# Kernel tuning notes

Measured on AMD Instinct MI355X. Metric: run time of the kernel, lower is better.

The kernel has to match this reference:

```python
import jax, jax.numpy as jnp
import numpy as np

BN_EPS = 1e-5


def setup_inputs() -> dict:
    key = jax.random.key(0)
    ks = jax.random.split(key, 16)
    B, n, m, C1, C2 = 8, 8192, 2048, 256, 256
    Cin, H1, H2 = C1 + C2, 512, 512
    inp = {
        'unknown': jax.random.uniform(ks[0], (B, n, 3), jnp.float32),
        'known': jax.random.uniform(ks[1], (B, m, 3), jnp.float32),
        'unknow_feats': jax.random.normal(ks[2], (B, C1, n), jnp.float32),
        'known_feats': jax.random.normal(ks[3], (B, C2, m), jnp.float32),
        # shared-MLP layer 1: Conv2d(512 -> 512, k=1, bias=False) + BN + ReLU
        'W1': jax.random.normal(ks[4], (H1, Cin), jnp.float32) * (1.0 / np.sqrt(Cin)),
        'g1': jax.random.uniform(ks[5], (H1,), jnp.float32, 0.5, 1.5),
        'b1': jax.random.normal(ks[6], (H1,), jnp.float32) * 0.1,
        'm1': jax.random.normal(ks[7], (H1,), jnp.float32) * 0.1,
        'v1': jax.random.uniform(ks[8], (H1,), jnp.float32, 0.5, 1.5),
        # shared-MLP layer 2
        'W2': jax.random.normal(ks[9], (H2, H1), jnp.float32) * (1.0 / np.sqrt(H1)),
        'g2': jax.random.uniform(ks[10], (H2,), jnp.float32, 0.5, 1.5),
        'b2': jax.random.normal(ks[11], (H2,), jnp.float32) * 0.1,
        'm2': jax.random.normal(ks[12], (H2,), jnp.float32) * 0.1,
        'v2': jax.random.uniform(ks[13], (H2,), jnp.float32, 0.5, 1.5),
    }
    return inp


def three_nn(unknown, known):
    # brute-force squared L2 distances (CUDA kernel returns squared dists)
    d2 = jnp.sum((unknown[:, :, None, :] - known[:, None, :, :]) ** 2, axis=-1)  # (B,n,m)
    neg_d, idx = jax.lax.top_k(-d2, 3)  # 3 smallest
    return -neg_d, idx  # (B,n,3), (B,n,3)


def three_interpolate(feats, idx, weight):
    # feats (B,C,m), idx (B,n,3), weight (B,n,3) -> (B,C,n)
    def _one(f, i, w):
        return jnp.einsum('cnk,nk->cn', f[:, i], w)
    return jax.vmap(_one)(feats, idx, weight)


def _conv_bn_relu(x, W, g, b, mu, var):
    # x (B,Cin,n) -> (B,Cout,n); 1x1 conv + inference BatchNorm + ReLU
    y = jnp.einsum('oc,bcn->bon', W, x)
    scale = g / jnp.sqrt(var + BN_EPS)
    y = y * scale[None, :, None] + (b - mu * scale)[None, :, None]
    return jax.nn.relu(y)


def reference(unknown, known, unknow_feats, known_feats,
              W1, g1, b1, m1, v1, W2, g2, b2, m2, v2):
    dist, idx = three_nn(unknown, known)
    dist_recip = 1.0 / (dist + 1e-8)
    weight = dist_recip / jnp.sum(dist_recip, axis=2, keepdims=True)
    new_features = three_interpolate(known_feats, idx, weight)  # (B,C2,n)
    new_features = jnp.concatenate([new_features, unknow_feats], axis=1)  # (B,C1+C2,n)
    h = _conv_bn_relu(new_features, W1, g1, b1, m1, v1)
    out = _conv_bn_relu(h, W2, g2, b2, m2, v2)
    return out  # (B, 512, n)
```

## Files before the change

kernel.cpp:

```cpp
#include <hip/hip_runtime.h>

typedef __bf16 bf16_t;
typedef __bf16 bf16x8 __attribute__((ext_vector_type(8)));
typedef float f32x4 __attribute__((ext_vector_type(4)));

#define AS1 __attribute__((address_space(1)))
#define AS3 __attribute__((address_space(3)))

__device__ __forceinline__ void gload_lds16(const void* g, void* l) {
    __builtin_amdgcn_global_load_lds((const AS1 unsigned int*)g,
                                     (AS3 unsigned int*)l, 16, 0, 0);
}

__device__ __forceinline__ unsigned int pack2(float a, float b) {
    unsigned short lo = __builtin_bit_cast(unsigned short, (bf16_t)a);
    unsigned short hi = __builtin_bit_cast(unsigned short, (bf16_t)b);
    return (unsigned int)lo | ((unsigned int)hi << 16);
}

__global__ __launch_bounds__(256) void prep_all(
    const float* __restrict__ W1, const float* __restrict__ W2,
    bf16_t* __restrict__ Wc1, bf16_t* __restrict__ Wc2,
    const float* g1, const float* b1, const float* m1, const float* v1,
    const float* g2, const float* b2, const float* m2, const float* v2,
    float* s1, float* t1, float* s2, float* t2)
{
    const int bx = blockIdx.x;
    if (bx < 1024) {
        size_t i = (size_t)bx * 256 + threadIdx.x;
        Wc1[i] = (bf16_t)W1[i];
    } else if (bx < 2048) {
        size_t i = (size_t)(bx - 1024) * 256 + threadIdx.x;
        Wc2[i] = (bf16_t)W2[i];
    } else {
#pragma unroll
        for (int k = 0; k < 2; ++k) {
            int i = threadIdx.x + k * 256;
            float s = __fdiv_rn(g1[i], __fsqrt_rn(__fadd_rn(v1[i], 1e-5f)));
            s1[i] = s;
            t1[i] = __fsub_rn(b1[i], __fmul_rn(m1[i], s));
            float q = __fdiv_rn(g2[i], __fsqrt_rn(__fadd_rn(v2[i], 1e-5f)));
            s2[i] = q;
            t2[i] = __fsub_rn(b2[i], __fmul_rn(m2[i], q));
        }
    }
}

__device__ __forceinline__ void insdi(float d, int i,
                                      float& D1, int& I1, float& D2, int& I2,
                                      float& D3, int& I3) {
    const bool q1 = d < D1, q2 = d < D2, q3 = d < D3;
    I3 = q2 ? I2 : (q3 ? i : I3);
    I2 = q1 ? I1 : (q2 ? i : I2);
    I1 = q1 ? i : I1;
    D3 = __builtin_amdgcn_fmed3f(d, D2, D3);
    D2 = __builtin_amdgcn_fmed3f(d, D1, D2);
    D1 = fminf(d, D1);
}

__global__ __launch_bounds__(256) void knn3_kernel(
    const float* __restrict__ unknown, const float* __restrict__ known,
    int* __restrict__ idx3, float* __restrict__ w3)
{
    __shared__ float md[4][64][3];
    __shared__ int   mi[4][64][3];
    const int b = blockIdx.y;
    const int tid = threadIdx.x;
    const int lane = tid & 63;
    const int wv = __builtin_amdgcn_readfirstlane(tid >> 6);

    const int p = blockIdx.x * 64 + lane;
    const size_t qo = ((size_t)b * 8192 + p) * 3;
    const float qx = unknown[qo + 0];
    const float qy = unknown[qo + 1];
    const float qz = unknown[qo + 2];

    const float* kp = known + (size_t)b * 2048 * 3 + (size_t)wv * 512 * 3;
    const int jb = wv * 512;

    float d1[4], d2[4], d3[4];
    int   i1[4], i2[4], i3[4];
#pragma unroll
    for (int c = 0; c < 4; ++c) {
        d1[c] = 1e30f; d2[c] = 1e30f; d3[c] = 1e30f;
        i1[c] = 0;     i2[c] = 0;     i3[c] = 0;
    }

#pragma unroll 2
    for (int t = 0; t < 128; ++t) {
#pragma unroll
        for (int c = 0; c < 4; ++c) {
            const int jl = c * 128 + t;
            const float kx = kp[jl * 3 + 0];
            const float ky = kp[jl * 3 + 1];
            const float kz = kp[jl * 3 + 2];
            float dx = __fsub_rn(qx, kx);
            float dy = __fsub_rn(qy, ky);
            float dz = __fsub_rn(qz, kz);
            float d = __fadd_rn(__fadd_rn(__fmul_rn(dx, dx), __fmul_rn(dy, dy)),
                                __fmul_rn(dz, dz));
            insdi(d, jb + jl, d1[c], i1[c], d2[c], i2[c], d3[c], i3[c]);
        }
    }
    float D1 = d1[0], D2 = d2[0], D3 = d3[0];
    int   I1 = i1[0], I2 = i2[0], I3 = i3[0];
#pragma unroll
    for (int c = 1; c < 4; ++c) {
        insdi(d1[c], i1[c], D1, I1, D2, I2, D3, I3);
        insdi(d2[c], i2[c], D1, I1, D2, I2, D3, I3);
        insdi(d3[c], i3[c], D1, I1, D2, I2, D3, I3);
    }
    md[wv][lane][0] = D1; md[wv][lane][1] = D2; md[wv][lane][2] = D3;
    mi[wv][lane][0] = I1; mi[wv][lane][1] = I2; mi[wv][lane][2] = I3;
    __syncthreads();

    if (tid < 64) {
        float F1 = md[0][tid][0], F2 = md[0][tid][1], F3 = md[0][tid][2];
        int   J1 = mi[0][tid][0], J2 = mi[0][tid][1], J3 = mi[0][tid][2];
#pragma unroll
        for (int w = 1; w < 4; ++w) {
            insdi(md[w][tid][0], mi[w][tid][0], F1, J1, F2, J2, F3, J3);
            insdi(md[w][tid][1], mi[w][tid][1], F1, J1, F2, J2, F3, J3);
            insdi(md[w][tid][2], mi[w][tid][2], F1, J1, F2, J2, F3, J3);
        }
        float r1 = __fdiv_rn(1.f, __fadd_rn(F1, 1e-8f));
        float r2 = __fdiv_rn(1.f, __fadd_rn(F2, 1e-8f));
        float r3 = __fdiv_rn(1.f, __fadd_rn(F3, 1e-8f));
        float s = __fadd_rn(__fadd_rn(r1, r2), r3);
        const int pp = blockIdx.x * 64 + tid;
        const size_t o = ((size_t)b * 8192 + pp) * 3;
        idx3[o + 0] = J1; idx3[o + 1] = J2; idx3[o + 2] = J3;
        w3[o + 0] = __fdiv_rn(r1, s);
        w3[o + 1] = __fdiv_rn(r2, s);
        w3[o + 2] = __fdiv_rn(r3, s);
    }
}

__global__ __launch_bounds__(256) void transpose_kf(
    const float* __restrict__ kf, float* __restrict__ kfT)
{
    __shared__ float tile[32][33];
    const int b = blockIdx.z;
    const int m0 = blockIdx.x * 32;
    const int c0 = blockIdx.y * 32;
    const int tx = threadIdx.x & 31;
    const int ty = threadIdx.x >> 5;
#pragma unroll
    for (int k = 0; k < 4; ++k) {
        const int c = c0 + ty + k * 8;
        tile[ty + k * 8][tx] = kf[((size_t)b * 256 + c) * 2048 + m0 + tx];
    }
    __syncthreads();
#pragma unroll
    for (int k = 0; k < 4; ++k) {
        const int m = m0 + ty + k * 8;
        kfT[((size_t)b * 2048 + m) * 256 + c0 + tx] = tile[tx][ty + k * 8];
    }
}

__global__ __launch_bounds__(256) void interp_uf(
    const float* __restrict__ kfT, const int* __restrict__ idx3,
    const float* __restrict__ w3, const float* __restrict__ uf,
    bf16_t* __restrict__ XT, int b0, int p0, int P)
{
    __shared__ bf16_t tile[64][66];
    const int bl = blockIdx.y;
    const int bg = b0 + bl;
    const int gsplit = P >> 4;

    if ((int)blockIdx.x < gsplit) {
        const int pt = blockIdx.x * 16 + (threadIdx.x >> 4);
        const int ch = (threadIdx.x & 15) * 16;
        const int p = p0 + pt;

        const size_t ib = ((size_t)bg * 8192 + p) * 3;
        const int i0 = idx3[ib + 0] & 2047;
        const int i1 = idx3[ib + 1] & 2047;
        const int i2 = idx3[ib + 2] & 2047;
        const float w0 = w3[ib + 0], w1 = w3[ib + 1], w2 = w3[ib + 2];

        const float4* r0 = (const float4*)(kfT + ((size_t)bg * 2048 + i0) * 256 + ch);
        const float4* r1 = (const float4*)(kfT + ((size_t)bg * 2048 + i1) * 256 + ch);
        const float4* r2 = (const float4*)(kfT + ((size_t)bg * 2048 + i2) * 256 + ch);

        unsigned int u[8];
#pragma unroll
        for (int q = 0; q < 4; ++q) {
            float4 a = r0[q], bv = r1[q], c = r2[q];
            float v0 = w0 * a.x + w1 * bv.x + w2 * c.x;
            float v1 = w0 * a.y + w1 * bv.y + w2 * c.y;
            float v2 = w0 * a.z + w1 * bv.z + w2 * c.z;
            float v3 = w0 * a.w + w1 * bv.w + w2 * c.w;
            u[q * 2 + 0] = pack2(v0, v1);
            u[q * 2 + 1] = pack2(v2, v3);
        }
        uint4* dst = (uint4*)(XT + ((size_t)bl * P + pt) * 512 + ch);
        dst[0] = make_uint4(u[0], u[1], u[2], u[3]);
        dst[1] = make_uint4(u[4], u[5], u[6], u[7]);
    } else {
        const int u2 = blockIdx.x - gsplit;
        const int c0 = (u2 & 3) * 64;
        const int pc = (u2 >> 2) * 64;
        const int tid = threadIdx.x;
        const int pl = tid & 63;
        const int grp = tid >> 6;
        const int p = p0 + pc + pl;

#pragma unroll
        for (int cc = 0; cc < 16; ++cc) {
            const int lc = grp * 16 + cc;
            tile[lc][pl] = (bf16_t)uf[((size_t)bg * 256 + c0 + lc) * 8192 + p];
        }
        __syncthreads();

        const int pr = tid >> 2;
        const int cs = (tid & 3) * 16;
        unsigned int u[8];
#pragma unroll
        for (int q = 0; q < 8; ++q) {
            unsigned short lo = __builtin_bit_cast(unsigned short, tile[cs + 2 * q + 0][pr]);
            unsigned short hi = __builtin_bit_cast(unsigned short, tile[cs + 2 * q + 1][pr]);
            u[q] = (unsigned int)lo | ((unsigned int)hi << 16);
        }
        uint4* dst = (uint4*)(XT + ((size_t)bl * P + pc + pr) * 512 + 256 + c0 + cs);
        dst[0] = make_uint4(u[0], u[1], u[2], u[3]);
        dst[1] = make_uint4(u[4], u[5], u[6], u[7]);
    }
}

template <bool CHAN_IS_M, bool F32_OUT>
__global__ __launch_bounds__(256) void gemm_bt_bn_relu(
    const bf16_t* __restrict__ A, const bf16_t* __restrict__ BT,
    void* __restrict__ Cv,
    const float* __restrict__ scale, const float* __restrict__ shift,
    int ldC, size_t strideA, size_t strideB, size_t strideC, size_t cofs)
{
    __shared__ __align__(16) bf16_t As[128 * 32];
    __shared__ __align__(16) bf16_t Bs[128 * 32];

    const int b = blockIdx.z;
    const int m0 = blockIdx.y * 128;
    const int n0 = blockIdx.x * 128;
    const bf16_t* Ab = A + (size_t)b * strideA + (size_t)m0 * 512;
    const bf16_t* Bb = BT + (size_t)b * strideB + (size_t)n0 * 512;
    const size_t cbase = cofs + (size_t)b * strideC;

    const int tid = threadIdx.x;
    const int lane = tid & 63;
    const int wave = tid >> 6;
    const int wm = (wave & 1) * 64;
    const int wn = (wave >> 1) * 64;

    const int ch0 = tid, ch1 = tid + 256;
    const size_t ga0 = (size_t)(ch0 >> 2) * 512 + (size_t)(ch0 & 3) * 8;
    const size_t ga1 = (size_t)(ch1 >> 2) * 512 + (size_t)(ch1 & 3) * 8;

    const int row_a = lane & 15;
    const int koff = (lane >> 4) * 8;

    f32x4 acc[4][4] = {};

    for (int kt = 0; kt < 512; kt += 32) {
        gload_lds16(Ab + ga0 + kt, As + (size_t)ch0 * 8);
        gload_lds16(Ab + ga1 + kt, As + (size_t)ch1 * 8);
        gload_lds16(Bb + ga0 + kt, Bs + (size_t)ch0 * 8);
        gload_lds16(Bb + ga1 + kt, Bs + (size_t)ch1 * 8);
        __builtin_amdgcn_s_waitcnt(0);
        __syncthreads();

        bf16x8 af[4], bfr[4];
#pragma unroll
        for (int i = 0; i < 4; ++i)
            af[i] = *(const bf16x8*)(As + (size_t)(wm + i * 16 + row_a) * 32 + koff);
#pragma unroll
        for (int j = 0; j < 4; ++j)
            bfr[j] = *(const bf16x8*)(Bs + (size_t)(wn + j * 16 + row_a) * 32 + koff);
#pragma unroll
        for (int i = 0; i < 4; ++i)
#pragma unroll
            for (int j = 0; j < 4; ++j)
                acc[i][j] = __builtin_amdgcn_mfma_f32_16x16x32_bf16(
                    af[i], bfr[j], acc[i][j], 0, 0, 0);
        __syncthreads();
    }

    const int col = lane & 15;
    const int rbase = (lane >> 4) * 4;
#pragma unroll
    for (int i = 0; i < 4; ++i) {
#pragma unroll
        for (int j = 0; j < 4; ++j) {
            const int mb = m0 + wm + i * 16 + rbase;
            const int nn = n0 + wn + j * 16 + col;
            float sc = 0.f, sh = 0.f;
            if (!CHAN_IS_M) { sc = scale[nn]; sh = shift[nn]; }
#pragma unroll
            for (int r = 0; r < 4; ++r) {
                const int mm = mb + r;
                float s = CHAN_IS_M ? scale[mm] : sc;
                float t = CHAN_IS_M ? shift[mm] : sh;
                float v = fmaxf(acc[i][j][r] * s + t, 0.0f);
                const size_t ci = cbase + (size_t)mm * (size_t)ldC + nn;
                if (F32_OUT) ((float*)Cv)[ci] = v;
                else         ((bf16_t*)Cv)[ci] = (bf16_t)v;
            }
        }
    }
}

extern "C" void kernel_launch(void* const* d_in, const int* in_sizes, int n_in,
                              void* d_out, int out_size, void* d_ws, size_t ws_size,
                              hipStream_t stream) {
    (void)in_sizes; (void)n_in; (void)out_size;
    const float* unknown  = (const float*)d_in[0];
    const float* known    = (const float*)d_in[1];
    const float* unknow_f = (const float*)d_in[2];
    const float* known_f  = (const float*)d_in[3];
    const float* W1       = (const float*)d_in[4];
    const float* g1 = (const float*)d_in[5]; const float* b1 = (const float*)d_in[6];
    const float* m1 = (const float*)d_in[7]; const float* v1 = (const float*)d_in[8];
    const float* W2       = (const float*)d_in[9];
    const float* g2 = (const float*)d_in[10]; const float* b2 = (const float*)d_in[11];
    const float* m2 = (const float*)d_in[12]; const float* v2 = (const float*)d_in[13];

    char* ws = (char*)d_ws;
    float* s1 = (float*)(ws + 0);
    float* t1 = s1 + 512;
    float* s2 = s1 + 1024;
    float* t2 = s1 + 1536;
    int*    idx3 = (int*)(ws + 16384);
    float*  w3   = (float*)(ws + 16384 + 786432);
    bf16_t* Wc1  = (bf16_t*)(ws + 1589248);
    bf16_t* Wc2  = (bf16_t*)(ws + 2113536);
    float*  kfT  = (float*)(ws + (3u << 20));
    const size_t FIXED = 20u << 20;

    size_t avail = (ws_size > FIXED) ? (ws_size - FIXED) : 0;
    size_t pts = avail / 2048;
    int nb, P;
    if (pts >= 65536)      { nb = 8; P = 8192; }
    else if (pts >= 8192)  { nb = (int)(pts / 8192); P = 8192; }
    else {
        nb = 1;
        P = (int)((pts / 128) * 128);
        if (P < 128) P = 128;
        if (P > 8192) P = 8192;
    }
    bf16_t* XT = (bf16_t*)(ws + FIXED);
    bf16_t* HT = XT + (size_t)nb * P * 512;

    prep_all<<<2049, 256, 0, stream>>>(W1, W2, Wc1, Wc2,
                                       g1, b1, m1, v1, g2, b2, m2, v2,
                                       s1, t1, s2, t2);
    knn3_kernel<<<dim3(128, 8), 256, 0, stream>>>(unknown, known, idx3, w3);
    transpose_kf<<<dim3(64, 8, 8), 256, 0, stream>>>(known_f, kfT);

    for (int b0 = 0; b0 < 8; b0 += nb) {
        const int cur = (8 - b0 < nb) ? (8 - b0) : nb;
        for (int p0 = 0; p0 < 8192; p0 += P) {
            const int cp = (8192 - p0 < P) ? (8192 - p0) : P;

            interp_uf<<<dim3(cp / 8, cur), 256, 0, stream>>>(
                kfT, idx3, w3, unknow_f, XT, b0, p0, cp);

            gemm_bt_bn_relu<false, false><<<dim3(4, cp / 128, cur), 256, 0, stream>>>(
                XT, Wc1, HT, s1, t1, 512,
                (size_t)cp * 512, (size_t)0, (size_t)cp * 512, (size_t)0);

            gemm_bt_bn_relu<true, true><<<dim3(cp / 128, 4, cur), 256, 0, stream>>>(
                Wc2, HT, d_out, s2, t2, 8192,
                (size_t)0, (size_t)cp * 512, (size_t)512 * 8192,
                (size_t)b0 * 512 * 8192 + p0);
        }
    }
}
```

Measured before the change: 449.2 us.

## Fuse preprocessing kernels, stage known points in LDS, swizzle GEMM LDS layout

Measured after the change: 419.1 us. -6.7%, faster.

```diff
diff --git a/kernel.cpp b/kernel.cpp
--- a/kernel.cpp
+++ b/kernel.cpp
@@ -16,34 +16,6 @@
     unsigned short lo = __builtin_bit_cast(unsigned short, (bf16_t)a);
     unsigned short hi = __builtin_bit_cast(unsigned short, (bf16_t)b);
     return (unsigned int)lo | ((unsigned int)hi << 16);
-}
-
-__global__ __launch_bounds__(256) void prep_all(
-    const float* __restrict__ W1, const float* __restrict__ W2,
-    bf16_t* __restrict__ Wc1, bf16_t* __restrict__ Wc2,
-    const float* g1, const float* b1, const float* m1, const float* v1,
-    const float* g2, const float* b2, const float* m2, const float* v2,
-    float* s1, float* t1, float* s2, float* t2)
-{
-    const int bx = blockIdx.x;
-    if (bx < 1024) {
-        size_t i = (size_t)bx * 256 + threadIdx.x;
-        Wc1[i] = (bf16_t)W1[i];
-    } else if (bx < 2048) {
-        size_t i = (size_t)(bx - 1024) * 256 + threadIdx.x;
-        Wc2[i] = (bf16_t)W2[i];
-    } else {
-#pragma unroll
-        for (int k = 0; k < 2; ++k) {
-            int i = threadIdx.x + k * 256;
-            float s = __fdiv_rn(g1[i], __fsqrt_rn(__fadd_rn(v1[i], 1e-5f)));
-            s1[i] = s;
-            t1[i] = __fsub_rn(b1[i], __fmul_rn(m1[i], s));
-            float q = __fdiv_rn(g2[i], __fsqrt_rn(__fadd_rn(v2[i], 1e-5f)));
-            s2[i] = q;
-            t2[i] = __fsub_rn(b2[i], __fmul_rn(m2[i], q));
-        }
-    }
 }
 
 __device__ __forceinline__ void insdi(float d, int i,
@@ -58,103 +30,141 @@
     D1 = fminf(d, D1);
 }
 
-__global__ __launch_bounds__(256) void knn3_kernel(
+__global__ __launch_bounds__(512) void phase0(
     const float* __restrict__ unknown, const float* __restrict__ known,
-    int* __restrict__ idx3, float* __restrict__ w3)
+    int* __restrict__ idx3, float* __restrict__ w3,
+    const float* __restrict__ kf, float* __restrict__ kfT,
+    const float* __restrict__ W1, const float* __restrict__ W2,
+    bf16_t* __restrict__ Wc1, bf16_t* __restrict__ Wc2,
+    const float* g1, const float* b1, const float* m1, const float* v1,
+    const float* g2, const float* b2, const float* m2, const float* v2,
+    float* s1, float* t1, float* s2, float* t2)
 {
-    __shared__ float md[4][64][3];
-    __shared__ int   mi[4][64][3];
-    const int b = blockIdx.y;
+    __shared__ __align__(16) char smem[45056];
+    const int bx = blockIdx.x;
     const int tid = threadIdx.x;
-    const int lane = tid & 63;
-    const int wv = __builtin_amdgcn_readfirstlane(tid >> 6);
-
-    const int p = blockIdx.x * 64 + lane;
-    const size_t qo = ((size_t)b * 8192 + p) * 3;
-    const float qx = unknown[qo + 0];
-    const float qy = unknown[qo + 1];
-    const float qz = unknown[qo + 2];
-
-    const float* kp = known + (size_t)b * 2048 * 3 + (size_t)wv * 512 * 3;
-    const int jb = wv * 512;
-
-    float d1[4], d2[4], d3[4];
-    int   i1[4], i2[4], i3[4];
-#pragma unroll
-    for (int c = 0; c < 4; ++c) {
-        d1[c] = 1e30f; d2[c] = 1e30f; d3[c] = 1e30f;
-        i1[c] = 0;     i2[c] = 0;     i3[c] = 0;
-    }
-
+
+    if (bx < 1024) {
+        float4* kp = (float4*)smem;
+        float (*md)[64][3] = (float(*)[64][3])(smem + 32768);
+        int   (*mi)[64][3] = (int(*)[64][3])(smem + 32768 + 6144);
+        const int b = bx >> 7;
+        const int px = bx & 127;
+        const int lane = tid & 63;
+        const int wv = tid >> 6;
+
+        const size_t kb = (size_t)b * 2048 * 3;
+        for (int t = tid; t < 2048; t += 512) {
+            kp[t] = make_float4(known[kb + t * 3 + 0], known[kb + t * 3 + 1],
+                                known[kb + t * 3 + 2], 0.f);
+        }
+        __syncthreads();
+
+        const int p = px * 64 + lane;
+        const size_t qo = ((size_t)b * 8192 + p) * 3;
+        const float qx = unknown[qo + 0];
+        const float qy = unknown[qo + 1];
+        const float qz = unknown[qo + 2];
+
+        float d1[4], d2[4], d3[4];
+        int   i1[4], i2[4], i3[4];
+#pragma unroll
+        for (int c = 0; c < 4; ++c) {
+            d1[c] = 1e30f; d2[c] = 1e30f; d3[c] = 1e30f;
+            i1[c] = 0;     i2[c] = 0;     i3[c] = 0;
+        }
+
+        const int jb = wv * 256;
 #pragma unroll 2
-    for (int t = 0; t < 128; ++t) {
-#pragma unroll
-        for (int c = 0; c < 4; ++c) {
-            const int jl = c * 128 + t;
-            const float kx = kp[jl * 3 + 0];
-            const float ky = kp[jl * 3 + 1];
-            const float kz = kp[jl * 3 + 2];
-            float dx = __fsub_rn(qx, kx);
-            float dy = __fsub_rn(qy, ky);
-            float dz = __fsub_rn(qz, kz);
-            float d = __fadd_rn(__fadd_rn(__fmul_rn(dx, dx), __fmul_rn(dy, dy)),
-                                __fmul_rn(dz, dz));
-            insdi(d, jb + jl, d1[c], i1[c], d2[c], i2[c], d3[c], i3[c]);
-        }
-    }
-    float D1 = d1[0], D2 = d2[0], D3 = d3[0];
-    int   I1 = i1[0], I2 = i2[0], I3 = i3[0];
-#pragma unroll
-    for (int c = 1; c < 4; ++c) {
-        insdi(d1[c], i1[c], D1, I1, D2, I2, D3, I3);
-        insdi(d2[c], i2[c], D1, I1, D2, I2, D3, I3);
-        insdi(d3[c], i3[c], D1, I1, D2, I2, D3, I3);
-    }
-    md[wv][lane][0] = D1; md[wv][lane][1] = D2; md[wv][lane][2] = D3;
-    mi[wv][lane][0] = I1; mi[wv][lane][1] = I2; mi[wv][lane][2] = I3;
-    __syncthreads();
-
-    if (tid < 64) {
-        float F1 = md[0][tid][0], F2 = md[0][tid][1], F3 = md[0][tid][2];
-        int   J1 = mi[0][tid][0], J2 = mi[0][tid][1], J3 = mi[0][tid][2];
-#pragma unroll
-        for (int w = 1; w < 4; ++w) {
-            insdi(md[w][tid][0], mi[w][tid][0], F1, J1, F2, J2, F3, J3);
-            insdi(md[w][tid][1], mi[w][tid][1], F1, J1, F2, J2, F3, J3);
-            insdi(md[w][tid][2], mi[w][tid][2], F1, J1, F2, J2, F3, J3);
-        }
-        float r1 = __fdiv_rn(1.f, __fadd_rn(F1, 1e-8f));
-        float r2 = __fdiv_rn(1.f, __fadd_rn(F2, 1e-8f));
-        float r3 = __fdiv_rn(1.f, __fadd_rn(F3, 1e-8f));
-        float s = __fadd_rn(__fadd_rn(r1, r2), r3);
-        const int pp = blockIdx.x * 64 + tid;
-        const size_t o = ((size_t)b * 8192 + pp) * 3;
-        idx3[o + 0] = J1; idx3[o + 1] = J2; idx3[o + 2] = J3;
-        w3[o + 0] = __fdiv_rn(r1, s);
-        w3[o + 1] = __fdiv_rn(r2, s);
-        w3[o + 2] = __fdiv_rn(r3, s);
-    }
-}
-
-__global__ __launch_bounds__(256) void transpose_kf(
-    const float* __restrict__ kf, float* __restrict__ kfT)
-{
-    __shared__ float tile[32][33];
-    const int b = blockIdx.z;
-    const int m0 = blockIdx.x * 32;
-    const int c0 = blockIdx.y * 32;
-    const int tx = threadIdx.x & 31;
-    const int ty = threadIdx.x >> 5;
-#pragma unroll
-    for (int k = 0; k < 4; ++k) {
-        const int c = c0 + ty + k * 8;
-        tile[ty + k * 8][tx] = kf[((size_t)b * 256 + c) * 2048 + m0 + tx];
-    }
-    __syncthreads();
-#pragma unroll
-    for (int k = 0; k < 4; ++k) {
-        const int m = m0 + ty + k * 8;
-        kfT[((size_t)b * 2048 + m) * 256 + c0 + tx] = tile[tx][ty + k * 8];
+        for (int t = 0; t < 64; ++t) {
+#pragma unroll
+            for (int c = 0; c < 4; ++c) {
+                const int j = jb + c * 64 + t;
+                float4 k = kp[j];
+                float dx = __fsub_rn(qx, k.x);
+                float dy = __fsub_rn(qy, k.y);
+                float dz = __fsub_rn(qz, k.z);
+                float d = __fadd_rn(__fadd_rn(__fmul_rn(dx, dx),
+                                              __fmul_rn(dy, dy)),
+                                    __fmul_rn(dz, dz));
+                insdi(d, j, d1[c], i1[c], d2[c], i2[c], d3[c], i3[c]);
+            }
+        }
+        float D1 = d1[0], D2 = d2[0], D3 = d3[0];
+        int   I1 = i1[0], I2 = i2[0], I3 = i3[0];
+#pragma unroll
+        for (int c = 1; c < 4; ++c) {
+            insdi(d1[c], i1[c], D1, I1, D2, I2, D3, I3);
+            insdi(d2[c], i2[c], D1, I1, D2, I2, D3, I3);
+            insdi(d3[c], i3[c], D1, I1, D2, I2, D3, I3);
+        }
+        md[wv][lane][0] = D1; md[wv][lane][1] = D2; md[wv][lane][2] = D3;
+        mi[wv][lane][0] = I1; mi[wv][lane][1] = I2; mi[wv][lane][2] = I3;
+        __syncthreads();
+
+        if (tid < 64) {
+            float F1 = md[0][tid][0], F2 = md[0][tid][1], F3 = md[0][tid][2];
+            int   J1 = mi[0][tid][0], J2 = mi[0][tid][1], J3 = mi[0][tid][2];
+#pragma unroll
+            for (int w = 1; w < 8; ++w) {
+                insdi(md[w][tid][0], mi[w][tid][0], F1, J1, F2, J2, F3, J3);
+                insdi(md[w][tid][1], mi[w][tid][1], F1, J1, F2, J2, F3, J3);
+                insdi(md[w][tid][2], mi[w][tid][2], F1, J1, F2, J2, F3, J3);
+            }
+            float r1 = __fdiv_rn(1.f, __fadd_rn(F1, 1e-8f));
+            float r2 = __fdiv_rn(1.f, __fadd_rn(F2, 1e-8f));
+            float r3 = __fdiv_rn(1.f, __fadd_rn(F3, 1e-8f));
+            float s = __fadd_rn(__fadd_rn(r1, r2), r3);
+            const int pp = px * 64 + tid;
+            const size_t o = ((size_t)b * 8192 + pp) * 3;
+            idx3[o + 0] = J1; idx3[o + 1] = J2; idx3[o + 2] = J3;
+            w3[o + 0] = __fdiv_rn(r1, s);
+            w3[o + 1] = __fdiv_rn(r2, s);
+            w3[o + 2] = __fdiv_rn(r3, s);
+        }
+    } else if (bx < 3072) {
+        float (*tile)[32][33] = (float(*)[32][33])smem;
+        const int u = bx - 1024;
+        const int b = u >> 8;
+        const int rem = u & 255;
+        const int ct = rem >> 5;
+        const int mt2 = rem & 31;
+        const int s = tid >> 8;
+        const int t = tid & 255;
+        const int m0 = (mt2 * 2 + s) * 32;
+        const int c0 = ct * 32;
+        const int tx = t & 31;
+        const int ty = t >> 5;
+#pragma unroll
+        for (int k = 0; k < 4; ++k) {
+            const int c = c0 + ty + k * 8;
+            tile[s][ty + k * 8][tx] = kf[((size_t)b * 256 + c) * 2048 + m0 + tx];
+        }
+        __syncthreads();
+#pragma unroll
+        for (int k = 0; k < 4; ++k) {
+            const int m = m0 + ty + k * 8;
+            kfT[((size_t)b * 2048 + m) * 256 + c0 + tx] = tile[s][tx][ty + k * 8];
+        }
+    } else if (bx < 3328) {
+        const int v = bx - 3072;
+        const float* Wsrc = (v < 128) ? W1 : W2;
+        bf16_t* Wdst = (v < 128) ? Wc1 : Wc2;
+        const size_t base = ((size_t)(v & 127) * 512 + tid) * 4;
+        float4 w = *(const float4*)(Wsrc + base);
+        unsigned int u0 = pack2(w.x, w.y);
+        unsigned int u1 = pack2(w.z, w.w);
+        *(uint2*)(Wdst + base) = make_uint2(u0, u1);
+    } else {
+        int i = tid;
+        if (i < 512) {
+            float s = __fdiv_rn(g1[i], __fsqrt_rn(__fadd_rn(v1[i], 1e-5f)));
+            s1[i] = s;
+            t1[i] = __fsub_rn(b1[i], __fmul_rn(m1[i], s));
+            float q = __fdiv_rn(g2[i], __fsqrt_rn(__fadd_rn(v2[i], 1e-5f)));
+            s2[i] = q;
+            t2[i] = __fsub_rn(b2[i], __fmul_rn(m2[i], q));
+        }
     }
 }
 
@@ -228,7 +238,7 @@
     }
 }
 
-template <bool CHAN_IS_M, bool F32_OUT>
+template <bool CHAN_IS_M, bool F32_OUT, int LT>
 __global__ __launch_bounds__(256) void gemm_bt_bn_relu(
     const bf16_t* __restrict__ A, const bf16_t* __restrict__ BT,
     void* __restrict__ Cv,
@@ -239,10 +249,6 @@
     __shared__ __align__(16) bf16_t Bs[128 * 32];
 
     const int b = blockIdx.z;
-    const int m0 = blockIdx.y * 128;
-    const int n0 = blockIdx.x * 128;
-    const bf16_t* Ab = A + (size_t)b * strideA + (size_t)m0 * 512;
-    const bf16_t* Bb = BT + (size_t)b * strideB + (size_t)n0 * 512;
     const size_t cbase = cofs + (size_t)b * strideC;
 
     const int tid = threadIdx.x;
@@ -252,57 +258,67 @@
     const int wn = (wave >> 1) * 64;
 
     const int ch0 = tid, ch1 = tid + 256;
-    const size_t ga0 = (size_t)(ch0 >> 2) * 512 + (size_t)(ch0 & 3) * 8;
-    const size_t ga1 = (size_t)(ch1 >> 2) * 512 + (size_t)(ch1 & 3) * 8;
+    const int row0 = ch0 >> 2, row1 = ch1 >> 2;
+    const size_t ga0 = (size_t)row0 * 512 + (size_t)((ch0 & 3) ^ ((row0 >> 1) & 3)) * 8;
+    const size_t ga1 = (size_t)row1 * 512 + (size_t)((ch1 & 3) ^ ((row1 >> 1) & 3)) * 8;
 
     const int row_a = lane & 15;
-    const int koff = (lane >> 4) * 8;
-
-    f32x4 acc[4][4] = {};
-
-    for (int kt = 0; kt < 512; kt += 32) {
-        gload_lds16(Ab + ga0 + kt, As + (size_t)ch0 * 8);
-        gload_lds16(Ab + ga1 + kt, As + (size_t)ch1 * 8);
-        gload_lds16(Bb + ga0 + kt, Bs + (size_t)ch0 * 8);
-        gload_lds16(Bb + ga1 + kt, Bs + (size_t)ch1 * 8);
-        __builtin_amdgcn_s_waitcnt(0);
-        __syncthreads();
-
-        bf16x8 af[4], bfr[4];
-#pragma unroll
-        for (int i = 0; i < 4; ++i)
-            af[i] = *(const bf16x8*)(As + (size_t)(wm + i * 16 + row_a) * 32 + koff);
-#pragma unroll
-        for (int j = 0; j < 4; ++j)
-            bfr[j] = *(const bf16x8*)(Bs + (size_t)(wn + j * 16 + row_a) * 32 + koff);
-#pragma unroll
-        for (int i = 0; i < 4; ++i)
-#pragma unroll
-            for (int j = 0; j < 4; ++j)
-                acc[i][j] = __builtin_amdgcn_mfma_f32_16x16x32_bf16(
-                    af[i], bfr[j], acc[i][j], 0, 0, 0);
-        __syncthreads();
-    }
-
+    const int kq = lane >> 4;
+    const int sw = (row_a >> 1) & 3;
+    const int kswz = (kq ^ sw) * 8;
     const int col = lane & 15;
     const int rbase = (lane >> 4) * 4;
-#pragma unroll
-    for (int i = 0; i < 4; ++i) {
-#pragma unroll
-        for (int j = 0; j < 4; ++j) {
-            const int mb = m0 + wm + i * 16 + rbase;
-            const int nn = n0 + wn + j * 16 + col;
-            float sc = 0.f, sh = 0.f;
-            if (!CHAN_IS_M) { sc = scale[nn]; sh = shift[nn]; }
-#pragma unroll
-            for (int r = 0; r < 4; ++r) {
-                const int mm = mb + r;
-                float s = CHAN_IS_M ? scale[mm] : sc;
-                float t = CHAN_IS_M ? shift[mm] : sh;
-                float v = fmaxf(acc[i][j][r] * s + t, 0.0f);
-                const size_t ci = cbase + (size_t)mm * (size_t)ldC + nn;
-                if (F32_OUT) ((float*)Cv)[ci] = v;
-                else         ((bf16_t*)Cv)[ci] = (bf16_t)v;
+
+    for (int lt = 0; lt < LT; ++lt) {
+        const int m0 = CHAN_IS_M ? (blockIdx.y * LT + lt) * 128 : blockIdx.y * 128;
+        const int n0 = CHAN_IS_M ? blockIdx.x * 128 : (blockIdx.x * LT + lt) * 128;
+        const bf16_t* Ab = A + (size_t)b * strideA + (size_t)m0 * 512;
+        const bf16_t* Bb = BT + (size_t)b * strideB + (size_t)n0 * 512;
+
+        f32x4 acc[4][4] = {};
+
+        for (int kt = 0; kt < 512; kt += 32) {
+            gload_lds16(Ab + ga0 + kt, As + (size_t)ch0 * 8);
+            gload_lds16(Ab + ga1 + kt, As + (size_t)ch1 * 8);
+            gload_lds16(Bb + ga0 + kt, Bs + (size_t)ch0 * 8);
+            gload_lds16(Bb + ga1 + kt, Bs + (size_t)ch1 * 8);
+            __builtin_amdgcn_s_waitcnt(0);
+            __syncthreads();
+
+            bf16x8 af[4], bfr[4];
+#pragma unroll
+            for (int i = 0; i < 4; ++i)
+                af[i] = *(const bf16x8*)(As + (size_t)(wm + i * 16 + row_a) * 32 + kswz);
+#pragma unroll
+            for (int j = 0; j < 4; ++j)
+                bfr[j] = *(const bf16x8*)(Bs + (size_t)(wn + j * 16 + row_a) * 32 + kswz);
+#pragma unroll
+            for (int i = 0; i < 4; ++i)
+#pragma unroll
+                for (int j = 0; j < 4; ++j)
+                    acc[i][j] = __builtin_amdgcn_mfma_f32_16x16x32_bf16(
+                        af[i], bfr[j], acc[i][j], 0, 0, 0);
+            __syncthreads();
+        }
+
+#pragma unroll
+        for (int i = 0; i < 4; ++i) {
+#pragma unroll
+            for (int j = 0; j < 4; ++j) {
+                const int mb = m0 + wm + i * 16 + rbase;
+                const int nn = n0 + wn + j * 16 + col;
+                float sc = 0.f, sh = 0.f;
+                if (!CHAN_IS_M) { sc = scale[nn]; sh = shift[nn]; }
+#pragma unroll
+                for (int r = 0; r < 4; ++r) {
+                    const int mm = mb + r;
+                    float s = CHAN_IS_M ? scale[mm] : sc;
+                    float t = CHAN_IS_M ? shift[mm] : sh;
+                    float v = fmaxf(acc[i][j][r] * s + t, 0.0f);
+                    const size_t ci = cbase + (size_t)mm * (size_t)ldC + nn;
+                    if (F32_OUT) ((float*)Cv)[ci] = v;
+                    else         ((bf16_t*)Cv)[ci] = (bf16_t)v;
+                }
             }
         }
     }
@@ -349,11 +365,10 @@
     bf16_t* XT = (bf16_t*)(ws + FIXED);
     bf16_t* HT = XT + (size_t)nb * P * 512;
 
-    prep_all<<<2049, 256, 0, stream>>>(W1, W2, Wc1, Wc2,
-                                       g1, b1, m1, v1, g2, b2, m2, v2,
-                                       s1, t1, s2, t2);
-    knn3_kernel<<<dim3(128, 8), 256, 0, stream>>>(unknown, known, idx3, w3);
-    transpose_kf<<<dim3(64, 8, 8), 256, 0, stream>>>(known_f, kfT);
+    phase0<<<3329, 512, 0, stream>>>(unknown, known, idx3, w3,
+                                     known_f, kfT, W1, W2, Wc1, Wc2,
+                                     g1, b1, m1, v1, g2, b2, m2, v2,
+                                     s1, t1, s2, t2);
 
     for (int b0 = 0; b0 < 8; b0 += nb) {
         const int cur = (8 - b0 < nb) ? (8 - b0) : nb;
@@ -363,11 +378,11 @@
             interp_uf<<<dim3(cp / 8, cur), 256, 0, stream>>>(
                 kfT, idx3, w3, unknow_f, XT, b0, p0, cp);
 
-            gemm_bt_bn_relu<false, false><<<dim3(4, cp / 128, cur), 256, 0, stream>>>(
+            gemm_bt_bn_relu<false, false, 2><<<dim3(2, cp / 128, cur), 256, 0, stream>>>(
                 XT, Wc1, HT, s1, t1, 512,
                 (size_t)cp * 512, (size_t)0, (size_t)cp * 512, (size_t)0);
 
-            gemm_bt_bn_relu<true, true><<<dim3(cp / 128, 4, cur), 256, 0, stream>>>(
+            gemm_bt_bn_relu<true, true, 2><<<dim3(cp / 128, 2, cur), 256, 0, stream>>>(
                 Wc2, HT, d_out, s2, t2, 8192,
                 (size_t)0, (size_t)cp * 512, (size_t)512 * 8192,
                 (size_t)b0 * 512 * 8192 + p0);
```
